# Optimization experiments

Hardware: AMD Instinct MI355X
Metric: run time of the kernel (lower is better)

## Reference

```python
import jax, jax.numpy as jnp
import numpy as np

N = 100_000   # nodes
E = 1_600_000 # directed edges
G = 2048      # graphs in batch
NF = 78       # input node features
DIM = 32      # GIN hidden dim
L = 5         # num GIN layers
OUT = 128     # output_dim
BN_EPS = 1e-5


def setup_inputs() -> dict:
    key = jax.random.key(0)
    ks = jax.random.split(key, 8)
    s = 0.1
    return {
        "x": jax.random.normal(ks[0], (N, NF), jnp.float32),
        "edge_index": jax.random.randint(ks[1], (2, E), 0, N, jnp.int32),
        "batch": jnp.sort(jax.random.randint(ks[2], (N,), 0, G, jnp.int32)),
        "W1_0": (jax.random.normal(ks[3], (NF, DIM), jnp.float32) * s),
        "W1_rest": (jax.random.normal(ks[4], (L - 1, DIM, DIM), jnp.float32) * s),
        "b1": jnp.zeros((L, DIM), jnp.float32),
        "W2": (jax.random.normal(ks[5], (L, DIM, DIM), jnp.float32) * s),
        "b2": jnp.zeros((L, DIM), jnp.float32),
        "gamma": jnp.ones((L, DIM), jnp.float32),
        "beta": jnp.zeros((L, DIM), jnp.float32),
        "Wfc": (jax.random.normal(ks[6], (DIM, OUT), jnp.float32) * s),
        "bfc": jnp.zeros((OUT,), jnp.float32),
    }


def reference(x, edge_index, batch, W1_0, W1_rest, b1, W2, b2, gamma, beta, Wfc, bfc):
    src, dst = edge_index[0], edge_index[1]
    h = x
    for i in range(L):
        # GINConv (eps=0): h_i' = MLP(h_i + sum_{j->i} h_j)
        agg = jax.ops.segment_sum(h[src], dst, num_segments=N)  # [N, d]
        h = h + agg
        W1 = W1_0 if i == 0 else W1_rest[i - 1]
        h = jnp.maximum(h @ W1 + b1[i], 0.0) @ W2[i] + b2[i]
        # ReLU then BatchNorm1d (training mode: batch stats, biased var)
        h = jnp.maximum(h, 0.0)
        mu = h.mean(axis=0)
        var = h.var(axis=0)
        h = gamma[i] * (h - mu) * jax.lax.rsqrt(var + BN_EPS) + beta[i]
    pooled = jax.ops.segment_sum(h, batch, num_segments=G)  # global_add_pool [G, DIM]
    return jnp.maximum(pooled @ Wfc + bfc, 0.0)  # dropout is identity (eval)
```

## Files before the change

kernel.cpp:

```cpp
#include <hip/hip_runtime.h>
#include <hip/hip_fp16.h>

#define N_NODES 100000
#define N_EDGES 1600000
#define N_GRAPHS 2048
#define NFEAT 78
#define DIM 32
#define NLAYERS 5
#define OUTD 128
#define BN_EPS 1e-5f
#define NPB 32
#define NBUK 391
#define BNODES 256
#define STRIDE 4608
#define EPB 4096
#define NBLK ((N_EDGES + EPB - 1) / EPB)
#define NSLOT 16
#define PSTRIDE (NSLOT * 2 * DIM)
#define OSTR (BNODES + 1)

__device__ __forceinline__ float2 up2(unsigned u) {
    __half2 h = *reinterpret_cast<__half2*>(&u);
    return __half22float2(h);
}
__device__ __forceinline__ unsigned pk2(float a, float b) {
    __half2 h = __floats2half2_rn(a, b);
    return *reinterpret_cast<unsigned*>(&h);
}

__global__ __launch_bounds__(256) void prep_kernel(
    const int* __restrict__ ei, int* __restrict__ bcnt, int* __restrict__ bdata,
    const float* __restrict__ x, const float* __restrict__ W1_0,
    unsigned short* __restrict__ y)
{
    __shared__ int cur[NBUK];
    __shared__ int gbl[NBUK];
    __shared__ float Wl[NFEAT * DIM];
    int tid = threadIdx.x;

    if (blockIdx.x < NBLK) {
        int base = blockIdx.x * EPB;
        for (int i = tid; i < NBUK; i += 256) cur[i] = 0;
        __syncthreads();

        int ew[16], eb[16];
        const int4* s4 = (const int4*)ei;
        const int4* d4 = (const int4*)(ei + N_EDGES);
#pragma unroll
        for (int c = 0; c < 4; ++c) {
            int eidx = base + c * 1024 + tid * 4;
            if (eidx < N_EDGES) {
                int4 sv = s4[eidx >> 2];
                int4 dv = d4[eidx >> 2];
                ew[c*4+0] = sv.x | ((dv.x & 255) << 17); eb[c*4+0] = dv.x >> 8;
                ew[c*4+1] = sv.y | ((dv.y & 255) << 17); eb[c*4+1] = dv.y >> 8;
                ew[c*4+2] = sv.z | ((dv.z & 255) << 17); eb[c*4+2] = dv.z >> 8;
                ew[c*4+3] = sv.w | ((dv.w & 255) << 17); eb[c*4+3] = dv.w >> 8;
            } else {
                eb[c*4+0] = eb[c*4+1] = eb[c*4+2] = eb[c*4+3] = -1;
                ew[c*4+0] = ew[c*4+1] = ew[c*4+2] = ew[c*4+3] = 0;
            }
        }
        int slot[16];
#pragma unroll
        for (int k = 0; k < 16; ++k)
            slot[k] = (eb[k] >= 0) ? atomicAdd(&cur[eb[k]], 1) : 0;
        __syncthreads();
        for (int b = tid; b < NBUK; b += 256) {
            int c = cur[b];
            gbl[b] = (c > 0) ? atomicAdd(&bcnt[b], c) : 0;
        }
        __syncthreads();
#pragma unroll
        for (int k = 0; k < 16; ++k) {
            int b = eb[k];
            if (b >= 0) {
                int pos = gbl[b] + slot[k];
                if (pos < STRIDE) bdata[b * STRIDE + pos] = ew[k];
            }
        }
    } else {
        for (int i = tid; i < NFEAT * DIM; i += 256) Wl[i] = W1_0[i];
        __syncthreads();
        int t = (blockIdx.x - NBLK) * 256 + tid;
        int row = t >> 3;
        int c0 = (t & 7) * 4;
        float a0 = 0.f, a1 = 0.f, a2 = 0.f, a3 = 0.f;
        const float* hr = x + (long)row * NFEAT;
        for (int k = 0; k < NFEAT; ++k) {
            float xv = hr[k];
            a0 = fmaf(xv, Wl[k * DIM + c0 + 0], a0);
            a1 = fmaf(xv, Wl[k * DIM + c0 + 1], a1);
            a2 = fmaf(xv, Wl[k * DIM + c0 + 2], a2);
            a3 = fmaf(xv, Wl[k * DIM + c0 + 3], a3);
        }
        ((uint2*)y)[(long)row * 8 + (t & 7)] = make_uint2(pk2(a0, a1), pk2(a2, a3));
    }
}

__global__ __launch_bounds__(256) void cfill2_kernel(
    const int* __restrict__ bcnt, const int* __restrict__ bdata,
    int* __restrict__ edge_src, int* __restrict__ offsB,
    int* __restrict__ ghist, int* __restrict__ gcursor)
{
    __shared__ int sorted[STRIDE];
    __shared__ int cnt[BNODES], off[BNODES], cur[BNODES];
    __shared__ int lhist[64];
    __shared__ int gbS;
    int b = blockIdx.x, tid = threadIdx.x;
    int n = min(bcnt[b], STRIDE);
    const int* slab = bdata + (long)b * STRIDE;

    if (tid == 0) gbS = atomicAdd(gcursor, n);
    if (tid < BNODES) cnt[tid] = 0;
    if (tid < 64) lhist[tid] = 0;
    __syncthreads();
    int gb = gbS;
    for (int i = tid; i < n; i += 256)
        atomicAdd(&cnt[slab[i] >> 17], 1);
    __syncthreads();
    int t = tid;
    if (t < BNODES) off[t] = cnt[t];
    __syncthreads();
    for (int o = 1; o < BNODES; o <<= 1) {
        int a = (t >= o && t < BNODES) ? off[t - o] : 0;
        __syncthreads();
        if (t < BNODES) off[t] += a;
        __syncthreads();
    }
    if (t < BNODES) {
        int excl = off[t] - cnt[t];
        off[t] = excl;
        cur[t] = excl;
        offsB[b * OSTR + t] = gb + excl;
        int node = b * BNODES + t;
        if (node < N_NODES) atomicAdd(&lhist[min(cnt[t], 63)], 1);
    }
    if (tid == 0) offsB[b * OSTR + BNODES] = gb + n;
    __syncthreads();
    if (tid < 64) {
        int h = lhist[tid];
        if (h) atomicAdd(&ghist[tid], h);
    }
    for (int i = tid; i < n; i += 256) {
        int w = slab[i];
        int pos = atomicAdd(&cur[w >> 17], 1);
        sorted[pos] = w & 0x1FFFF;
    }
    __syncthreads();
    for (int i = tid; i < n; i += 256)
        edge_src[gb + i] = sorted[i];
}

__global__ __launch_bounds__(64) void dscan_kernel(
    const int* __restrict__ ghist, int* __restrict__ binCursor)
{
    __shared__ int sd[64];
    int t = threadIdx.x;
    int v = ghist[t];
    sd[t] = v; __syncthreads();
    for (int off = 1; off < 64; off <<= 1) {
        int a = (t >= off) ? sd[t - off] : 0;
        __syncthreads();
        sd[t] += a;
        __syncthreads();
    }
    binCursor[t] = sd[t] - v;
}

__global__ __launch_bounds__(256) void dfill_kernel(
    const int* __restrict__ offsB, int* __restrict__ binCursor,
    int* __restrict__ perm)
{
    __shared__ int lhist[64], lbase[64], lcur[64];
    int tid = threadIdx.x;
    int node = blockIdx.x * 256 + tid;
    if (tid < 64) { lhist[tid] = 0; lcur[tid] = 0; }
    __syncthreads();
    int bin = -1;
    if (node < N_NODES) {
        int b = node >> 8, t = node & 255;
        int d = offsB[b * OSTR + t + 1] - offsB[b * OSTR + t];
        bin = min(d, 63);
        atomicAdd(&lhist[bin], 1);
    }
    __syncthreads();
    if (tid < 64) {
        int c = lhist[tid];
        lbase[tid] = c ? atomicAdd(&binCursor[tid], c) : 0;
    }
    __syncthreads();
    if (bin >= 0) {
        int p = atomicAdd(&lcur[bin], 1);
        perm[lbase[bin] + p] = node;
    }
}

template<bool MM>
__global__ __launch_bounds__(256) void layer_kernel(
    const int* __restrict__ perm,
    const int* __restrict__ offsB, const int* __restrict__ edge_src,
    const unsigned short* __restrict__ zin,
    const float* __restrict__ W1g,
    const float* __restrict__ partial_prev,
    const float* __restrict__ gprev, const float* __restrict__ bprev,
    const float* __restrict__ b1v,
    const float* __restrict__ W2, const float* __restrict__ b2v,
    unsigned short* __restrict__ zout, float* __restrict__ partial)
{
    __shared__ float W1l[DIM * DIM];
    __shared__ float W2l[DIM * DIM];
    __shared__ float zs[NPB][36];
    __shared__ float b1l[DIM], b2l[DIM], cl[DIM];
    __shared__ float sscl[DIM], sshl[DIM];
    __shared__ float psum[DIM], psq[DIM];

    int tid = threadIdx.x;
    float* red = &zs[0][0];

    for (int i = tid; i < DIM * DIM; i += 256) W2l[i] = W2[i];
    if (tid < DIM) {
        b1l[tid] = b1v[tid]; b2l[tid] = b2v[tid];
        psum[tid] = 0.f; psq[tid] = 0.f;
    }
    if (MM) {
        int c = tid & 63, chunk = tid >> 6;
        float a = 0.f;
        for (int p = chunk; p < NSLOT; p += 4) a += partial_prev[p * 64 + c];
        red[tid] = a;
        __syncthreads();
        if (tid < 64) red[tid] = red[tid] + red[tid+64] + red[tid+128] + red[tid+192];
        __syncthreads();
        if (tid < DIM) {
            const float invN = 1.0f / (float)N_NODES;
            float S = red[tid], Q = red[tid + DIM];
            float mu = S * invN;
            float var = Q * invN - mu * mu;
            float sc = gprev[tid] * rsqrtf(var + BN_EPS);
            sscl[tid] = sc;
            sshl[tid] = bprev[tid] - mu * sc;
        }
        __syncthreads();
        for (int i = tid; i < DIM * DIM; i += 256) W1l[i] = sscl[i >> 5] * W1g[i];
        if (tid < DIM) {
            float cv = 0.f;
            for (int k = 0; k < DIM; ++k) cv = fmaf(sshl[k], W1g[k * DIM + tid], cv);
            cl[tid] = cv;
        }
    }
    __syncthreads();

    int ln = tid >> 3, p = tid & 7;
    int c0 = p * 4;
    int node = perm[blockIdx.x * NPB + ln];
    int ob = (node >> 8) * OSTR + (node & 255);
    int beg = offsB[ob], end = offsB[ob + 1];
    int deg = end - beg;
    const uint2* zb = (const uint2*)zin;

    uint2 sv = zb[(long)node * 8 + p];
    float2 f;
    f = up2(sv.x); float a0 = f.x, a1 = f.y;
    f = up2(sv.y); float a2 = f.x, a3 = f.y;
    int e = beg;
    for (; e + 8 <= end; e += 8) {
        uint2 v0 = zb[(long)edge_src[e + 0] * 8 + p];
        uint2 v1 = zb[(long)edge_src[e + 1] * 8 + p];
        uint2 v2 = zb[(long)edge_src[e + 2] * 8 + p];
        uint2 v3 = zb[(long)edge_src[e + 3] * 8 + p];
        uint2 v4 = zb[(long)edge_src[e + 4] * 8 + p];
        uint2 v5 = zb[(long)edge_src[e + 5] * 8 + p];
        uint2 v6 = zb[(long)edge_src[e + 6] * 8 + p];
        uint2 v7 = zb[(long)edge_src[e + 7] * 8 + p];
        f = up2(v0.x); a0 += f.x; a1 += f.y;  f = up2(v0.y); a2 += f.x; a3 += f.y;
        f = up2(v1.x); a0 += f.x; a1 += f.y;  f = up2(v1.y); a2 += f.x; a3 += f.y;
        f = up2(v2.x); a0 += f.x; a1 += f.y;  f = up2(v2.y); a2 += f.x; a3 += f.y;
        f = up2(v3.x); a0 += f.x; a1 += f.y;  f = up2(v3.y); a2 += f.x; a3 += f.y;
        f = up2(v4.x); a0 += f.x; a1 += f.y;  f = up2(v4.y); a2 += f.x; a3 += f.y;
        f = up2(v5.x); a0 += f.x; a1 += f.y;  f = up2(v5.y); a2 += f.x; a3 += f.y;
        f = up2(v6.x); a0 += f.x; a1 += f.y;  f = up2(v6.y); a2 += f.x; a3 += f.y;
        f = up2(v7.x); a0 += f.x; a1 += f.y;  f = up2(v7.y); a2 += f.x; a3 += f.y;
    }
    for (; e < end; ++e) {
        uint2 v = zb[(long)edge_src[e] * 8 + p];
        f = up2(v.x); a0 += f.x; a1 += f.y;
        f = up2(v.y); a2 += f.x; a3 += f.y;
    }
    *(float4*)&zs[ln][c0] = make_float4(a0, a1, a2, a3);

    float t4[4];
    if (MM) {
        t4[0] = t4[1] = t4[2] = t4[3] = 0.f;
#pragma unroll
        for (int k = 0; k < DIM; ++k) {
            float zk = zs[ln][k];
            t4[0] = fmaf(zk, W1l[k * DIM + c0 + 0], t4[0]);
            t4[1] = fmaf(zk, W1l[k * DIM + c0 + 1], t4[1]);
            t4[2] = fmaf(zk, W1l[k * DIM + c0 + 2], t4[2]);
            t4[3] = fmaf(zk, W1l[k * DIM + c0 + 3], t4[3]);
        }
        float dp1 = (float)(deg + 1);
#pragma unroll
        for (int j = 0; j < 4; ++j)
            t4[j] = fmaxf(fmaf(dp1, cl[c0 + j], t4[j]) + b1l[c0 + j], 0.f);
    } else {
        t4[0] = fmaxf(a0 + b1l[c0 + 0], 0.f);
        t4[1] = fmaxf(a1 + b1l[c0 + 1], 0.f);
        t4[2] = fmaxf(a2 + b1l[c0 + 2], 0.f);
        t4[3] = fmaxf(a3 + b1l[c0 + 3], 0.f);
    }
    *(float4*)&zs[ln][c0] = make_float4(t4[0], t4[1], t4[2], t4[3]);

    float zv[4] = { b2l[c0 + 0], b2l[c0 + 1], b2l[c0 + 2], b2l[c0 + 3] };
#pragma unroll
    for (int k = 0; k < DIM; ++k) {
        float sk = zs[ln][k];
        zv[0] = fmaf(sk, W2l[k * DIM + c0 + 0], zv[0]);
        zv[1] = fmaf(sk, W2l[k * DIM + c0 + 1], zv[1]);
        zv[2] = fmaf(sk, W2l[k * DIM + c0 + 2], zv[2]);
        zv[3] = fmaf(sk, W2l[k * DIM + c0 + 3], zv[3]);
    }
#pragma unroll
    for (int j = 0; j < 4; ++j) zv[j] = fmaxf(zv[j], 0.f);
    ((uint2*)zout)[(long)node * 8 + p] = make_uint2(pk2(zv[0], zv[1]), pk2(zv[2], zv[3]));

    float sq[4];
#pragma unroll
    for (int j = 0; j < 4; ++j) sq[j] = zv[j] * zv[j];
#pragma unroll
    for (int off = 8; off < 64; off <<= 1) {
#pragma unroll
        for (int j = 0; j < 4; ++j) {
            zv[j] += __shfl_xor(zv[j], off, 64);
            sq[j] += __shfl_xor(sq[j], off, 64);
        }
    }
    if ((tid & 63) < 8) {
#pragma unroll
        for (int j = 0; j < 4; ++j) {
            atomicAdd(&psum[c0 + j], zv[j]);
            atomicAdd(&psq[c0 + j], sq[j]);
        }
    }
    __syncthreads();
    if (tid < 2 * DIM) {
        float v = (tid < DIM) ? psum[tid] : psq[tid - DIM];
        atomicAdd(&partial[(blockIdx.x & (NSLOT - 1)) * 2 * DIM + tid], v);
    }
}

__global__ __launch_bounds__(256) void pool_kernel(
    const unsigned short* __restrict__ z, const int* __restrict__ batch,
    float* __restrict__ praw, float* __restrict__ cntg)
{
    __shared__ float acc[32][32];
    __shared__ float cntL[32];
    __shared__ int slot[32];
    __shared__ int segg[32];
    __shared__ int nsegS;
    int tid = threadIdx.x;
    for (int i = tid; i < 1024; i += 256) ((float*)acc)[i] = 0.f;
    if (tid < 32) cntL[tid] = 0.f;
    int nodeBase = blockIdx.x * 32;
    if (tid < 32) {
        int nd = nodeBase + tid;
        int gv = batch[nd];
        int flag = (tid == 0) ? 1 : (gv != batch[nd - 1]);
        unsigned long long m = __ballot(flag);
        int s = __popcll(m & ((2ull << tid) - 1ull)) - 1;
        slot[tid] = s;
        if (flag) segg[s] = gv;
        if (tid == 0) nsegS = __popcll(m);
    }
    __syncthreads();

    int ln = tid >> 3;
    int p = tid & 7;
    long node = nodeBase + ln;
    uint2 u = ((const uint2*)z)[node * 8 + p];
    int c = p * 4;
    float2 f01 = up2(u.x), f23 = up2(u.y);
    int s = slot[ln];
    atomicAdd(&acc[s][c+0], f01.x);
    atomicAdd(&acc[s][c+1], f01.y);
    atomicAdd(&acc[s][c+2], f23.x);
    atomicAdd(&acc[s][c+3], f23.y);
    if (p == 0) atomicAdd(&cntL[s], 1.f);
    __syncthreads();

    int total = nsegS * 32;
    for (int i = tid; i < total; i += 256) {
        int r = i >> 5, dd = i & 31;
        float val = acc[r][dd];
        if (val != 0.f) atomicAdd(&praw[(long)segg[r] * DIM + dd], val);
    }
    if (tid < nsegS) atomicAdd(&cntg[segg[tid]], cntL[tid]);
}

__global__ __launch_bounds__(256) void fc_kernel(
    const float* __restrict__ praw, const float* __restrict__ cntg,
    const float* __restrict__ partial4,
    const float* __restrict__ g4, const float* __restrict__ be4,
    const float* __restrict__ Wfc, const float* __restrict__ bfc,
    float* __restrict__ out)
{
    __shared__ float Wl[DIM * OUTD];
    __shared__ float red[256];
    __shared__ float sscl[DIM], sshl[DIM], dvec[OUTD];
    int tid = threadIdx.x;
    for (int i = tid; i < DIM * OUTD; i += 256) Wl[i] = Wfc[i];
    {
        int c = tid & 63, chunk = tid >> 6;
        float a = 0.f;
        for (int p = chunk; p < NSLOT; p += 4) a += partial4[p * 64 + c];
        red[tid] = a;
    }
    __syncthreads();
    if (tid < 64) red[tid] = red[tid] + red[tid+64] + red[tid+128] + red[tid+192];
    __syncthreads();
    if (tid < DIM) {
        const float invN = 1.0f / (float)N_NODES;
        float S = red[tid], Q = red[tid + DIM];
        float mu = S * invN;
        float var = Q * invN - mu * mu;
        float sc = g4[tid] * rsqrtf(var + BN_EPS);
        sscl[tid] = sc;
        sshl[tid] = be4[tid] - mu * sc;
    }
    __syncthreads();
    if (tid < OUTD) {
        float dv = 0.f;
        for (int k = 0; k < DIM; ++k) dv = fmaf(sshl[k], Wl[k * OUTD + tid], dv);
        dvec[tid] = dv;
    }
    __syncthreads();
    int t = blockIdx.x * 256 + tid;
    int g = t >> 7;
    int o = t & (OUTD - 1);
    float acc = bfc[o] + cntg[g] * dvec[o];
    const float* pr = praw + (long)g * DIM;
#pragma unroll
    for (int k = 0; k < DIM; ++k)
        acc = fmaf(sscl[k] * pr[k], Wl[k * OUTD + o], acc);
    out[t] = fmaxf(acc, 0.f);
}

extern "C" void kernel_launch(void* const* d_in, const int* in_sizes, int n_in,
                              void* d_out, int out_size, void* d_ws, size_t ws_size,
                              hipStream_t stream) {
    const float* x      = (const float*)d_in[0];
    const int*   ei     = (const int*)  d_in[1];
    const int*   batch  = (const int*)  d_in[2];
    const float* W1_0   = (const float*)d_in[3];
    const float* W1_rest= (const float*)d_in[4];
    const float* b1     = (const float*)d_in[5];
    const float* W2     = (const float*)d_in[6];
    const float* b2     = (const float*)d_in[7];
    const float* gamma  = (const float*)d_in[8];
    const float* beta   = (const float*)d_in[9];
    const float* Wfc    = (const float*)d_in[10];
    const float* bfc    = (const float*)d_in[11];
    float* out = (float*)d_out;

    int* wsi = (int*)d_ws;
    const size_t nf = (size_t)N_NODES * DIM;
    const size_t BD = (size_t)NBUK * STRIDE;
    int*   bdata  = wsi;
    unsigned short* zfpA = (unsigned short*)(wsi + BD);
    unsigned short* zfpB = zfpA + nf;
    int*   edge_src = (int*)(zfpB + nf);
    int*   offsB  = edge_src + N_EDGES;
    int*   perm   = offsB + NBUK * OSTR;
    int*   bcnt   = perm + N_NODES;
    int*   ghist  = bcnt + NBUK;
    int*   gcursor= ghist + 64;
    int*   binCursor = gcursor + 1;
    float* praw   = (float*)(binCursor + 64);
    float* cntg   = praw + (size_t)N_GRAPHS * DIM;
    float* partial= cntg + N_GRAPHS;

    hipMemsetAsync(praw, 0,
        ((size_t)N_GRAPHS * DIM + N_GRAPHS + NLAYERS * PSTRIDE) * sizeof(float),
        stream);
    hipMemsetAsync(bcnt, 0, (size_t)(NBUK + 64 + 1) * sizeof(int), stream);

    const int grpBlocks = (N_NODES * 8) / 256;

    prep_kernel<<<NBLK + grpBlocks, 256, 0, stream>>>(
        ei, bcnt, bdata, x, W1_0, zfpA);
    cfill2_kernel<<<NBUK, 256, 0, stream>>>(
        bcnt, bdata, edge_src, offsB, ghist, gcursor);
    dscan_kernel<<<1, 64, 0, stream>>>(ghist, binCursor);
    dfill_kernel<<<(N_NODES + 255) / 256, 256, 0, stream>>>(offsB, binCursor, perm);

    layer_kernel<false><<<N_NODES / NPB, 256, 0, stream>>>(
        perm, offsB, edge_src, zfpA, nullptr, nullptr, nullptr, nullptr,
        b1, W2, b2, zfpB, partial);

    const unsigned short* zi = zfpB;
    unsigned short* zo = zfpA;
    for (int i = 1; i < NLAYERS; ++i) {
        layer_kernel<true><<<N_NODES / NPB, 256, 0, stream>>>(
            perm, offsB, edge_src, zi,
            W1_rest + (size_t)(i - 1) * DIM * DIM,
            partial + (size_t)(i - 1) * PSTRIDE,
            gamma + (i - 1) * DIM, beta + (i - 1) * DIM,
            b1 + i * DIM, W2 + (size_t)i * DIM * DIM, b2 + i * DIM,
            zo, partial + (size_t)i * PSTRIDE);
        const unsigned short* tmp = zi; zi = zo; zo = (unsigned short*)tmp;
    }

    pool_kernel<<<N_NODES / 32, 256, 0, stream>>>(zi, batch, praw, cntg);
    fc_kernel<<<(N_GRAPHS * OUTD) / 256, 256, 0, stream>>>(
        praw, cntg, partial + (size_t)(NLAYERS - 1) * PSTRIDE,
        gamma + (NLAYERS - 1) * DIM, beta + (NLAYERS - 1) * DIM,
        Wfc, bfc, out);
}
```

Baseline: 301.1 us.

## Replace global degree-bin node sort with per-window local degree sort

Drops the global degree histogram, its single-block scan kernel and the global bin-cursor fill. A new kernel sorts nodes by degree inside fixed 4096-node windows using a block-local histogram and wavefront shuffle scan. This removes one kernel launch and the global atomics, and keeps the node permutation local so gathers stay near the original node order. In exchange, load balancing is only per window, so layer blocks can see less uniform degree mixes.

```diff
diff --git a/kernel.cpp b/kernel.cpp
--- a/kernel.cpp
+++ b/kernel.cpp
@@ -18,6 +18,8 @@
 #define NSLOT 16
 #define PSTRIDE (NSLOT * 2 * DIM)
 #define OSTR (BNODES + 1)
+#define WIN 4096
+#define NWIN ((N_NODES + WIN - 1) / WIN)
 
 __device__ __forceinline__ float2 up2(unsigned u) {
     __half2 h = *reinterpret_cast<__half2*>(&u);
@@ -101,11 +103,10 @@
 __global__ __launch_bounds__(256) void cfill2_kernel(
     const int* __restrict__ bcnt, const int* __restrict__ bdata,
     int* __restrict__ edge_src, int* __restrict__ offsB,
-    int* __restrict__ ghist, int* __restrict__ gcursor)
+    int* __restrict__ gcursor)
 {
     __shared__ int sorted[STRIDE];
     __shared__ int cnt[BNODES], off[BNODES], cur[BNODES];
-    __shared__ int lhist[64];
     __shared__ int gbS;
     int b = blockIdx.x, tid = threadIdx.x;
     int n = min(bcnt[b], STRIDE);
@@ -113,7 +114,6 @@
 
     if (tid == 0) gbS = atomicAdd(gcursor, n);
     if (tid < BNODES) cnt[tid] = 0;
-    if (tid < 64) lhist[tid] = 0;
     __syncthreads();
     int gb = gbS;
     for (int i = tid; i < n; i += 256)
@@ -133,15 +133,9 @@
         off[t] = excl;
         cur[t] = excl;
         offsB[b * OSTR + t] = gb + excl;
-        int node = b * BNODES + t;
-        if (node < N_NODES) atomicAdd(&lhist[min(cnt[t], 63)], 1);
     }
     if (tid == 0) offsB[b * OSTR + BNODES] = gb + n;
     __syncthreads();
-    if (tid < 64) {
-        int h = lhist[tid];
-        if (h) atomicAdd(&ghist[tid], h);
-    }
     for (int i = tid; i < n; i += 256) {
         int w = slab[i];
         int pos = atomicAdd(&cur[w >> 17], 1);
@@ -152,47 +146,48 @@
         edge_src[gb + i] = sorted[i];
 }
 
-__global__ __launch_bounds__(64) void dscan_kernel(
-    const int* __restrict__ ghist, int* __restrict__ binCursor)
+__global__ __launch_bounds__(256) void wsort_kernel(
+    const int* __restrict__ offsB, int* __restrict__ perm)
 {
-    __shared__ int sd[64];
-    int t = threadIdx.x;
-    int v = ghist[t];
-    sd[t] = v; __syncthreads();
-    for (int off = 1; off < 64; off <<= 1) {
-        int a = (t >= off) ? sd[t - off] : 0;
-        __syncthreads();
-        sd[t] += a;
-        __syncthreads();
-    }
-    binCursor[t] = sd[t] - v;
-}
-
-__global__ __launch_bounds__(256) void dfill_kernel(
-    const int* __restrict__ offsB, int* __restrict__ binCursor,
-    int* __restrict__ perm)
-{
-    __shared__ int lhist[64], lbase[64], lcur[64];
+    __shared__ int hist[64], bbase[64], cur[64];
     int tid = threadIdx.x;
-    int node = blockIdx.x * 256 + tid;
-    if (tid < 64) { lhist[tid] = 0; lcur[tid] = 0; }
-    __syncthreads();
-    int bin = -1;
-    if (node < N_NODES) {
-        int b = node >> 8, t = node & 255;
-        int d = offsB[b * OSTR + t + 1] - offsB[b * OSTR + t];
-        bin = min(d, 63);
-        atomicAdd(&lhist[bin], 1);
+    int wbase = blockIdx.x * WIN;
+    int wn = min(WIN, N_NODES - wbase);
+    if (tid < 64) hist[tid] = 0;
+    __syncthreads();
+    int bins[WIN / 256];
+#pragma unroll
+    for (int k = 0; k < WIN / 256; ++k) {
+        int i = k * 256 + tid;
+        int bin = -1;
+        if (i < wn) {
+            int node = wbase + i;
+            int ob = (node >> 8) * OSTR + (node & 255);
+            bin = min(offsB[ob + 1] - offsB[ob], 63);
+            atomicAdd(&hist[bin], 1);
+        }
+        bins[k] = bin;
     }
     __syncthreads();
     if (tid < 64) {
-        int c = lhist[tid];
-        lbase[tid] = c ? atomicAdd(&binCursor[tid], c) : 0;
-    }
-    __syncthreads();
-    if (bin >= 0) {
-        int p = atomicAdd(&lcur[bin], 1);
-        perm[lbase[bin] + p] = node;
+        int v = hist[tid];
+        int s = v;
+        for (int off = 1; off < 64; off <<= 1) {
+            int a = __shfl_up(s, off, 64);
+            if ((tid & 63) >= off) s += a;
+        }
+        bbase[tid] = s - v;
+        cur[tid] = s - v;
+    }
+    __syncthreads();
+#pragma unroll
+    for (int k = 0; k < WIN / 256; ++k) {
+        int bin = bins[k];
+        if (bin >= 0) {
+            int node = wbase + k * 256 + tid;
+            int p = atomicAdd(&cur[bin], 1);
+            perm[wbase + p] = node;
+        }
     }
 }
 
@@ -472,26 +467,23 @@
     int*   offsB  = edge_src + N_EDGES;
     int*   perm   = offsB + NBUK * OSTR;
     int*   bcnt   = perm + N_NODES;
-    int*   ghist  = bcnt + NBUK;
-    int*   gcursor= ghist + 64;
-    int*   binCursor = gcursor + 1;
-    float* praw   = (float*)(binCursor + 64);
+    int*   gcursor= bcnt + NBUK;
+    float* praw   = (float*)(gcursor + 1);
     float* cntg   = praw + (size_t)N_GRAPHS * DIM;
     float* partial= cntg + N_GRAPHS;
 
     hipMemsetAsync(praw, 0,
         ((size_t)N_GRAPHS * DIM + N_GRAPHS + NLAYERS * PSTRIDE) * sizeof(float),
         stream);
-    hipMemsetAsync(bcnt, 0, (size_t)(NBUK + 64 + 1) * sizeof(int), stream);
+    hipMemsetAsync(bcnt, 0, (size_t)(NBUK + 1) * sizeof(int), stream);
 
     const int grpBlocks = (N_NODES * 8) / 256;
 
     prep_kernel<<<NBLK + grpBlocks, 256, 0, stream>>>(
         ei, bcnt, bdata, x, W1_0, zfpA);
     cfill2_kernel<<<NBUK, 256, 0, stream>>>(
-        bcnt, bdata, edge_src, offsB, ghist, gcursor);
-    dscan_kernel<<<1, 64, 0, stream>>>(ghist, binCursor);
-    dfill_kernel<<<(N_NODES + 255) / 256, 256, 0, stream>>>(offsB, binCursor, perm);
+        bcnt, bdata, edge_src, offsB, gcursor);
+    wsort_kernel<<<NWIN, 256, 0, stream>>>(offsB, perm);
 
     layer_kernel<false><<<N_NODES / NPB, 256, 0, stream>>>(
         perm, offsB, edge_src, zfpA, nullptr, nullptr, nullptr, nullptr,
```

Result: no change. 306.2 us (+1.7%).
